# Optimization experiments

Measured on AMD Instinct MI355X. Metric: run time of the kernel, lower is better.

The kernel has to match this reference:

```python
import jax, jax.numpy as jnp
import numpy as np

K = 0.1  # curvature (called k in the module)
EPS = 1e-15

def setup_inputs() -> dict:
    key = jax.random.key(0)
    k1, k2, k3 = jax.random.split(key, 3)
    B, C, D = 2048, 1000, 64
    x = jax.random.normal(k1, (B, D), dtype=jnp.float32) * 0.05  # inside ball
    a_vals = jax.random.normal(k2, (C, D), dtype=jnp.float32) * 0.05
    p_vals = jax.random.normal(k3, (C, D), dtype=jnp.float32) * 0.05
    return {"x": x, "a_vals": a_vals, "p_vals": p_vals}

def reference(x, a_vals, p_vals):
    k = jnp.asarray(K, dtype=x.dtype)
    sqrt_k = jnp.sqrt(k)
    # poincare_exp0: exponential map at the origin
    p_norm = jnp.maximum(jnp.linalg.norm(p_vals, axis=1, keepdims=True), EPS)  # [C,1]
    p_poin = jnp.tanh(sqrt_k * p_norm) * p_vals / (sqrt_k * p_norm)            # [C,D]
    # conformal scaling of a (as written in the module: 1 + k*||p||^2)
    p2 = jnp.sum(p_poin * p_poin, axis=1)                                      # [C]
    a_poin = a_vals * (1.0 + k * p2)[:, None]                                  # [C,D]
    # hyperbolic softmax logits
    lam = 2.0 / (1.0 - k * p2)                                                 # [C]
    a_norm = jnp.maximum(jnp.linalg.norm(a_poin, axis=1), EPS)                 # [C]
    scale = lam * a_norm / sqrt_k                                              # [C]
    # mobius addition of (-p) (+) x, batched -> [C,B,D]
    mp = -p_poin                                                               # [C,D]
    xy = jnp.einsum('cd,bd->cb', mp, x)                                        # [C,B]
    x2 = jnp.sum(mp * mp, axis=-1)[:, None]                                    # [C,1]
    y2 = jnp.sum(x * x, axis=-1)[None, :]                                      # [1,B]
    num = ((1.0 + 2.0 * k * xy + k * y2)[..., None] * mp[:, None, :]
           + (1.0 - k * x2)[..., None] * x[None, :, :])                        # [C,B,D]
    den = 1.0 + 2.0 * k * xy + (k * k) * x2 * y2                               # [C,B]
    mob = num / den[..., None]                                                 # [C,B,D]
    numer = 2.0 * sqrt_k * jnp.einsum('cbd,cd->cb', mob, a_poin)               # [C,B]
    denom = a_norm[:, None] * (1.0 - k * jnp.sum(mob * mob, axis=-1))          # [C,B]
    logits = scale[:, None] * jnp.arcsinh(numer / denom)                       # [C,B]
    return logits.T                                                            # [B,C]
```

## Files before the change

kernel.cpp:

```cpp
#include <hip/hip_runtime.h>
#include <hip/hip_bf16.h>
#include <math.h>

#define KCURV  0.1f
#define KK     0.010000001f
#define SQRT_K 0.31622776601683794f
#define TWO_SQRT_K 0.6324555320336759f
#define INV_SQRT_K 3.1622776601683795f
#define TD 64

typedef __bf16  bf16x8  __attribute__((ext_vector_type(8)));
typedef float   f32x4   __attribute__((ext_vector_type(4)));

__device__ __forceinline__ unsigned short f2bf(float f) {
    __hip_bfloat16 h = __float2bfloat16(f);
    return *(unsigned short*)&h;
}

__global__ __launch_bounds__(256) void prep_kernel(
    const float* __restrict__ a_vals, const float* __restrict__ p_vals,
    unsigned short* __restrict__ Pbf, unsigned short* __restrict__ Abf,
    float* __restrict__ x2g, float* __restrict__ pag,
    float* __restrict__ ang, float* __restrict__ scg,
    int C)
{
    const int tid  = threadIdx.x;
    const int item = blockIdx.x * 64 + (tid >> 2);
    const int q    = tid & 3;
    const int gc   = item < C ? item : C - 1;

    const float* pr = p_vals + (size_t)gc * TD + q * 16;
    const float* ar = a_vals + (size_t)gc * TD + q * 16;
    float pv[16], av[16];
    #pragma unroll
    for (int m = 0; m < 4; ++m) {
        *(float4*)&pv[m * 4] = *(const float4*)(pr + m * 4);
        *(float4*)&av[m * 4] = *(const float4*)(ar + m * 4);
    }
    float s_pp = 0.f, s_aa = 0.f, s_pa = 0.f;
    #pragma unroll
    for (int u = 0; u < 16; ++u) {
        s_pp = fmaf(pv[u], pv[u], s_pp);
        s_aa = fmaf(av[u], av[u], s_aa);
        s_pa = fmaf(pv[u], av[u], s_pa);
    }
    s_pp += __shfl_xor(s_pp, 1, 64); s_pp += __shfl_xor(s_pp, 2, 64);
    s_aa += __shfl_xor(s_aa, 1, 64); s_aa += __shfl_xor(s_aa, 2, 64);
    s_pa += __shfl_xor(s_pa, 1, 64); s_pa += __shfl_xor(s_pa, 2, 64);

    float pn = sqrtf(s_pp); if (pn < 1e-15f) pn = 1e-15f;
    float arg = SQRT_K * pn;
    float t = tanhf(arg);
    float factor = t / arg;
    float p2 = factor * factor * s_pp;
    float ca = 1.0f + KCURV * p2;
    float anorm = ca * sqrtf(s_aa); if (anorm < 1e-15f) anorm = 1e-15f;
    float lam = 2.0f / (1.0f - KCURV * p2);
    float scale = lam * anorm * INV_SQRT_K;
    float pa = -factor * ca * s_pa;

    if (q == 0) {
        x2g[item] = p2; pag[item] = pa; ang[item] = anorm; scg[item] = scale;
    }
    unsigned short ubp[16], uba[16];
    #pragma unroll
    for (int u = 0; u < 16; ++u) {
        ubp[u] = f2bf(-factor * pv[u]);
        uba[u] = f2bf(ca * av[u]);
    }
    unsigned short* dp = Pbf + (size_t)item * TD + q * 16;
    unsigned short* da = Abf + (size_t)item * TD + q * 16;
    *(ulonglong2*)dp       = *(const ulonglong2*)&ubp[0];
    *(ulonglong2*)(dp + 8) = *(const ulonglong2*)&ubp[8];
    *(ulonglong2*)da       = *(const ulonglong2*)&uba[0];
    *(ulonglong2*)(da + 8) = *(const ulonglong2*)&uba[8];
}

__global__ __launch_bounds__(256) void mlr_gemm_kernel(
    const float* __restrict__ x,
    const unsigned short* __restrict__ Pbf, const unsigned short* __restrict__ Abf,
    const float* __restrict__ x2g, const float* __restrict__ pag,
    const float* __restrict__ ang, const float* __restrict__ scg,
    float* __restrict__ out, int B, int C)
{
    const int tid  = threadIdx.x;
    const int w    = tid >> 6;
    const int lane = tid & 63;
    const int m16  = lane & 15;
    const int quad = lane >> 4;
    const int cb   = blockIdx.x * 64;
    const int rb   = blockIdx.y * 64;
    int arow = rb + 16 * w + m16; if (arow >= B) arow = B - 1;

    float xv[2][8];
    bf16x8 bp[4][2], ba[4][2];
    #pragma unroll
    for (int step = 0; step < 2; ++step) {
        const int ko = quad * 8 + step * 32;
        const float* xr = x + (size_t)arow * TD + ko;
        *(float4*)&xv[step][0] = *(const float4*)xr;
        *(float4*)&xv[step][4] = *(const float4*)(xr + 4);
        #pragma unroll
        for (int t = 0; t < 4; ++t) {
            const size_t crow = (size_t)(cb + 16 * t + m16) * TD + ko;
            bp[t][step] = *(const bf16x8*)(Pbf + crow);
            ba[t][step] = *(const bf16x8*)(Abf + crow);
        }
    }

    float s = 0.f;
    #pragma unroll
    for (int step = 0; step < 2; ++step)
        #pragma unroll
        for (int u = 0; u < 8; ++u) s = fmaf(xv[step][u], xv[step][u], s);
    s += __shfl_xor(s, 16, 64);
    s += __shfl_xor(s, 32, 64);
    float y2r[4];
    #pragma unroll
    for (int r = 0; r < 4; ++r) y2r[r] = __shfl(s, quad * 4 + r, 64);

    bf16x8 af[2];
    #pragma unroll
    for (int step = 0; step < 2; ++step) {
        union { unsigned short u[8]; bf16x8 v; } cv;
        #pragma unroll
        for (int u = 0; u < 8; ++u) cv.u[u] = f2bf(xv[step][u]);
        af[step] = cv.v;
    }

    f32x4 accP[4], accA[4];
    #pragma unroll
    for (int t = 0; t < 4; ++t) {
        accP[t] = (f32x4){0.f, 0.f, 0.f, 0.f};
        accA[t] = (f32x4){0.f, 0.f, 0.f, 0.f};
    }
    #pragma unroll
    for (int step = 0; step < 2; ++step) {
        #pragma unroll
        for (int t = 0; t < 4; ++t) {
            accP[t] = __builtin_amdgcn_mfma_f32_16x16x32_bf16(af[step], bp[t][step], accP[t], 0, 0, 0);
            accA[t] = __builtin_amdgcn_mfma_f32_16x16x32_bf16(af[step], ba[t][step], accA[t], 0, 0, 0);
        }
    }

    #pragma unroll
    for (int t = 0; t < 4; ++t) {
        const int cl = cb + 16 * t + m16;
        const float x2 = x2g[cl], pa = pag[cl], an = ang[cl], sc = scg[cl];
        const float beta = 1.0f - KCURV * x2;
        const float kkx2 = KK * x2;
        #pragma unroll
        for (int r = 0; r < 4; ++r) {
            const int gr = rb + 16 * w + quad * 4 + r;
            const float y2 = y2r[r];
            const float xy = accP[t][r];
            const float xa = accA[t][r];
            float t1    = fmaf(2.0f * KCURV, xy, 1.0f);
            float den   = fmaf(kkx2, y2, t1);
            float alpha = fmaf(KCURV, y2, t1);
            float g     = fmaf(alpha, pa, beta * xa);
            float M     = fmaf(alpha * alpha, x2,
                          fmaf(2.0f * alpha * beta, xy, beta * beta * y2));
            float dd    = fmaf(den, den, -KCURV * M);
            float z     = TWO_SQRT_K * g * den * __builtin_amdgcn_rcpf(an * dd);
            float lg    = sc * __logf(z + sqrtf(fmaf(z, z, 1.0f)));
            if (cl < C && gr < B) out[(size_t)gr * C + cl] = lg;
        }
    }
}

extern "C" void kernel_launch(void* const* d_in, const int* in_sizes, int n_in,
                              void* d_out, int out_size, void* d_ws, size_t ws_size,
                              hipStream_t stream) {
    const float* x      = (const float*)d_in[0];
    const float* a_vals = (const float*)d_in[1];
    const float* p_vals = (const float*)d_in[2];
    const int B = in_sizes[0] / TD;
    const int C = in_sizes[1] / TD;
    const int rowBlocks = (B + 63) / 64;
    const int clsBlocks = (C + 63) / 64;
    const int CPAD = clsBlocks * 64;

    char* ws = (char*)d_ws;
    unsigned short* Pbf = (unsigned short*)ws;
    unsigned short* Abf = (unsigned short*)(ws + (size_t)CPAD * TD * 2);
    float* x2g = (float*)(ws + (size_t)CPAD * TD * 4);
    float* pag = x2g + CPAD;
    float* ang = pag + CPAD;
    float* scg = ang + CPAD;

    prep_kernel<<<clsBlocks, 256, 0, stream>>>(
        a_vals, p_vals, Pbf, Abf, x2g, pag, ang, scg, C);

    dim3 grid(clsBlocks, rowBlocks);
    mlr_gemm_kernel<<<grid, dim3(256), 0, stream>>>(
        x, Pbf, Abf, x2g, pag, ang, scg, (float*)d_out, B, C);
}
```

Before: 69.68 us.

## Fuse class-parameter prep into GEMM kernel, dropping separate prep launch

Removes the prep kernel and has each GEMM block load fp32 p and a rows directly, computing norms, tanh scaling, per-class scalars and bf16 conversion in registers before the MFMAs. This eliminates one kernel launch and the workspace round-trip for bf16 copies and scalars. In exchange, the per-class prep work is redundantly recomputed by every row block (32x), and the blocks read twice as many bytes of fp32 input, with higher register pressure.

```diff
diff --git a/kernel.cpp b/kernel.cpp
--- a/kernel.cpp
+++ b/kernel.cpp
@@ -17,71 +17,9 @@
     return *(unsigned short*)&h;
 }
 
-__global__ __launch_bounds__(256) void prep_kernel(
-    const float* __restrict__ a_vals, const float* __restrict__ p_vals,
-    unsigned short* __restrict__ Pbf, unsigned short* __restrict__ Abf,
-    float* __restrict__ x2g, float* __restrict__ pag,
-    float* __restrict__ ang, float* __restrict__ scg,
-    int C)
-{
-    const int tid  = threadIdx.x;
-    const int item = blockIdx.x * 64 + (tid >> 2);
-    const int q    = tid & 3;
-    const int gc   = item < C ? item : C - 1;
-
-    const float* pr = p_vals + (size_t)gc * TD + q * 16;
-    const float* ar = a_vals + (size_t)gc * TD + q * 16;
-    float pv[16], av[16];
-    #pragma unroll
-    for (int m = 0; m < 4; ++m) {
-        *(float4*)&pv[m * 4] = *(const float4*)(pr + m * 4);
-        *(float4*)&av[m * 4] = *(const float4*)(ar + m * 4);
-    }
-    float s_pp = 0.f, s_aa = 0.f, s_pa = 0.f;
-    #pragma unroll
-    for (int u = 0; u < 16; ++u) {
-        s_pp = fmaf(pv[u], pv[u], s_pp);
-        s_aa = fmaf(av[u], av[u], s_aa);
-        s_pa = fmaf(pv[u], av[u], s_pa);
-    }
-    s_pp += __shfl_xor(s_pp, 1, 64); s_pp += __shfl_xor(s_pp, 2, 64);
-    s_aa += __shfl_xor(s_aa, 1, 64); s_aa += __shfl_xor(s_aa, 2, 64);
-    s_pa += __shfl_xor(s_pa, 1, 64); s_pa += __shfl_xor(s_pa, 2, 64);
-
-    float pn = sqrtf(s_pp); if (pn < 1e-15f) pn = 1e-15f;
-    float arg = SQRT_K * pn;
-    float t = tanhf(arg);
-    float factor = t / arg;
-    float p2 = factor * factor * s_pp;
-    float ca = 1.0f + KCURV * p2;
-    float anorm = ca * sqrtf(s_aa); if (anorm < 1e-15f) anorm = 1e-15f;
-    float lam = 2.0f / (1.0f - KCURV * p2);
-    float scale = lam * anorm * INV_SQRT_K;
-    float pa = -factor * ca * s_pa;
-
-    if (q == 0) {
-        x2g[item] = p2; pag[item] = pa; ang[item] = anorm; scg[item] = scale;
-    }
-    unsigned short ubp[16], uba[16];
-    #pragma unroll
-    for (int u = 0; u < 16; ++u) {
-        ubp[u] = f2bf(-factor * pv[u]);
-        uba[u] = f2bf(ca * av[u]);
-    }
-    unsigned short* dp = Pbf + (size_t)item * TD + q * 16;
-    unsigned short* da = Abf + (size_t)item * TD + q * 16;
-    *(ulonglong2*)dp       = *(const ulonglong2*)&ubp[0];
-    *(ulonglong2*)(dp + 8) = *(const ulonglong2*)&ubp[8];
-    *(ulonglong2*)da       = *(const ulonglong2*)&uba[0];
-    *(ulonglong2*)(da + 8) = *(const ulonglong2*)&uba[8];
-}
-
-__global__ __launch_bounds__(256) void mlr_gemm_kernel(
-    const float* __restrict__ x,
-    const unsigned short* __restrict__ Pbf, const unsigned short* __restrict__ Abf,
-    const float* __restrict__ x2g, const float* __restrict__ pag,
-    const float* __restrict__ ang, const float* __restrict__ scg,
-    float* __restrict__ out, int B, int C)
+__global__ __launch_bounds__(256) void mlr_fused_kernel(
+    const float* __restrict__ x, const float* __restrict__ a_vals,
+    const float* __restrict__ p_vals, float* __restrict__ out, int B, int C)
 {
     const int tid  = threadIdx.x;
     const int w    = tid >> 6;
@@ -92,27 +30,34 @@
     const int rb   = blockIdx.y * 64;
     int arow = rb + 16 * w + m16; if (arow >= B) arow = B - 1;
 
-    float xv[2][8];
-    bf16x8 bp[4][2], ba[4][2];
+    float xv[16];
+    {
+        const float* xr = x + (size_t)arow * TD + quad * 8;
+        *(float4*)&xv[0]  = *(const float4*)xr;
+        *(float4*)&xv[4]  = *(const float4*)(xr + 4);
+        *(float4*)&xv[8]  = *(const float4*)(xr + 32);
+        *(float4*)&xv[12] = *(const float4*)(xr + 36);
+    }
+
+    float pv[4][16], av[4][16];
     #pragma unroll
-    for (int step = 0; step < 2; ++step) {
-        const int ko = quad * 8 + step * 32;
-        const float* xr = x + (size_t)arow * TD + ko;
-        *(float4*)&xv[step][0] = *(const float4*)xr;
-        *(float4*)&xv[step][4] = *(const float4*)(xr + 4);
-        #pragma unroll
-        for (int t = 0; t < 4; ++t) {
-            const size_t crow = (size_t)(cb + 16 * t + m16) * TD + ko;
-            bp[t][step] = *(const bf16x8*)(Pbf + crow);
-            ba[t][step] = *(const bf16x8*)(Abf + crow);
-        }
+    for (int t = 0; t < 4; ++t) {
+        int cl = cb + 16 * t + m16; if (cl >= C) cl = C - 1;
+        const float* pr = p_vals + (size_t)cl * TD + quad * 8;
+        const float* ar = a_vals + (size_t)cl * TD + quad * 8;
+        *(float4*)&pv[t][0]  = *(const float4*)pr;
+        *(float4*)&pv[t][4]  = *(const float4*)(pr + 4);
+        *(float4*)&pv[t][8]  = *(const float4*)(pr + 32);
+        *(float4*)&pv[t][12] = *(const float4*)(pr + 36);
+        *(float4*)&av[t][0]  = *(const float4*)ar;
+        *(float4*)&av[t][4]  = *(const float4*)(ar + 4);
+        *(float4*)&av[t][8]  = *(const float4*)(ar + 32);
+        *(float4*)&av[t][12] = *(const float4*)(ar + 36);
     }
 
     float s = 0.f;
     #pragma unroll
-    for (int step = 0; step < 2; ++step)
-        #pragma unroll
-        for (int u = 0; u < 8; ++u) s = fmaf(xv[step][u], xv[step][u], s);
+    for (int u = 0; u < 16; ++u) s = fmaf(xv[u], xv[u], s);
     s += __shfl_xor(s, 16, 64);
     s += __shfl_xor(s, 32, 64);
     float y2r[4];
@@ -124,29 +69,63 @@
     for (int step = 0; step < 2; ++step) {
         union { unsigned short u[8]; bf16x8 v; } cv;
         #pragma unroll
-        for (int u = 0; u < 8; ++u) cv.u[u] = f2bf(xv[step][u]);
+        for (int u = 0; u < 8; ++u) cv.u[u] = f2bf(xv[step * 8 + u]);
         af[step] = cv.v;
     }
 
     f32x4 accP[4], accA[4];
+    float x2c[4], pac[4], anc[4], scc[4];
     #pragma unroll
     for (int t = 0; t < 4; ++t) {
-        accP[t] = (f32x4){0.f, 0.f, 0.f, 0.f};
-        accA[t] = (f32x4){0.f, 0.f, 0.f, 0.f};
-    }
-    #pragma unroll
-    for (int step = 0; step < 2; ++step) {
+        float s_pp = 0.f, s_aa = 0.f, s_pa = 0.f;
         #pragma unroll
-        for (int t = 0; t < 4; ++t) {
-            accP[t] = __builtin_amdgcn_mfma_f32_16x16x32_bf16(af[step], bp[t][step], accP[t], 0, 0, 0);
-            accA[t] = __builtin_amdgcn_mfma_f32_16x16x32_bf16(af[step], ba[t][step], accA[t], 0, 0, 0);
+        for (int u = 0; u < 16; ++u) {
+            s_pp = fmaf(pv[t][u], pv[t][u], s_pp);
+            s_aa = fmaf(av[t][u], av[t][u], s_aa);
+            s_pa = fmaf(pv[t][u], av[t][u], s_pa);
         }
+        s_pp += __shfl_xor(s_pp, 16, 64); s_pp += __shfl_xor(s_pp, 32, 64);
+        s_aa += __shfl_xor(s_aa, 16, 64); s_aa += __shfl_xor(s_aa, 32, 64);
+        s_pa += __shfl_xor(s_pa, 16, 64); s_pa += __shfl_xor(s_pa, 32, 64);
+
+        float pn = sqrtf(s_pp); if (pn < 1e-15f) pn = 1e-15f;
+        float arg = SQRT_K * pn;
+        float th = tanhf(arg);
+        float factor = th / arg;
+        float p2 = factor * factor * s_pp;
+        float ca = 1.0f + KCURV * p2;
+        float anorm = ca * sqrtf(s_aa); if (anorm < 1e-15f) anorm = 1e-15f;
+        float lam = 2.0f / (1.0f - KCURV * p2);
+        x2c[t] = p2;
+        pac[t] = -factor * ca * s_pa;
+        anc[t] = anorm;
+        scc[t] = lam * anorm * INV_SQRT_K;
+
+        bf16x8 bp[2], ba[2];
+        #pragma unroll
+        for (int step = 0; step < 2; ++step) {
+            union { unsigned short u[8]; bf16x8 v; } cp, cab;
+            #pragma unroll
+            for (int u = 0; u < 8; ++u) {
+                cp.u[u]  = f2bf(-factor * pv[t][step * 8 + u]);
+                cab.u[u] = f2bf(ca * av[t][step * 8 + u]);
+            }
+            bp[step] = cp.v; ba[step] = cab.v;
+        }
+
+        f32x4 zp = (f32x4){0.f, 0.f, 0.f, 0.f};
+        f32x4 za = (f32x4){0.f, 0.f, 0.f, 0.f};
+        zp = __builtin_amdgcn_mfma_f32_16x16x32_bf16(af[0], bp[0], zp, 0, 0, 0);
+        zp = __builtin_amdgcn_mfma_f32_16x16x32_bf16(af[1], bp[1], zp, 0, 0, 0);
+        za = __builtin_amdgcn_mfma_f32_16x16x32_bf16(af[0], ba[0], za, 0, 0, 0);
+        za = __builtin_amdgcn_mfma_f32_16x16x32_bf16(af[1], ba[1], za, 0, 0, 0);
+        accP[t] = zp; accA[t] = za;
     }
 
     #pragma unroll
     for (int t = 0; t < 4; ++t) {
         const int cl = cb + 16 * t + m16;
-        const float x2 = x2g[cl], pa = pag[cl], an = ang[cl], sc = scg[cl];
+        const float x2 = x2c[t], pa = pac[t], an = anc[t], sc = scc[t];
         const float beta = 1.0f - KCURV * x2;
         const float kkx2 = KK * x2;
         #pragma unroll
@@ -179,20 +158,8 @@
     const int C = in_sizes[1] / TD;
     const int rowBlocks = (B + 63) / 64;
     const int clsBlocks = (C + 63) / 64;
-    const int CPAD = clsBlocks * 64;
-
-    char* ws = (char*)d_ws;
-    unsigned short* Pbf = (unsigned short*)ws;
-    unsigned short* Abf = (unsigned short*)(ws + (size_t)CPAD * TD * 2);
-    float* x2g = (float*)(ws + (size_t)CPAD * TD * 4);
-    float* pag = x2g + CPAD;
-    float* ang = pag + CPAD;
-    float* scg = ang + CPAD;
-
-    prep_kernel<<<clsBlocks, 256, 0, stream>>>(
-        a_vals, p_vals, Pbf, Abf, x2g, pag, ang, scg, C);
 
     dim3 grid(clsBlocks, rowBlocks);
-    mlr_gemm_kernel<<<grid, dim3(256), 0, stream>>>(
-        x, Pbf, Abf, x2g, pag, ang, scg, (float*)d_out, B, C);
+    mlr_fused_kernel<<<grid, dim3(256), 0, stream>>>(
+        x, a_vals, p_vals, (float*)d_out, B, C);
 }
```

Measured after the change: 71.50 us. 2.6% more time.
